# Performance work log

Hardware: AMD Instinct MI355X
Metric: run time of the kernel (lower is better)

The kernel has to match this reference:

```python
import jax, jax.numpy as jnp
import numpy as np

N, E, F, H, C = 50000, 800000, 128, 256, 40
BN_EPS = 1e-5


def setup_inputs() -> dict:
    key = jax.random.key(0)
    ks = jax.random.split(key, 8)
    s = 0.05
    return {
        'x': jax.random.normal(ks[0], (N, F), jnp.float32),
        'edge_index': jax.random.randint(ks[1], (2, E), 0, N),
        'eps1': jnp.zeros((), jnp.float32),
        'W1': jax.random.normal(ks[2], (F, H), jnp.float32) * s,
        'b1': jnp.zeros((H,), jnp.float32),
        'g1': jnp.ones((H,), jnp.float32),
        'be1': jnp.zeros((H,), jnp.float32),
        'W2': jax.random.normal(ks[3], (H, H), jnp.float32) * s,
        'b2': jnp.zeros((H,), jnp.float32),
        'eps2': jnp.zeros((), jnp.float32),
        'W3': jax.random.normal(ks[4], (H, H), jnp.float32) * s,
        'b3': jnp.zeros((H,), jnp.float32),
        'g2': jnp.ones((H,), jnp.float32),
        'be2': jnp.zeros((H,), jnp.float32),
        'W4': jax.random.normal(ks[5], (H, H), jnp.float32) * s,
        'b4': jnp.zeros((H,), jnp.float32),
        'g3': jnp.ones((H,), jnp.float32),
        'be3': jnp.zeros((H,), jnp.float32),
        'Wf': jax.random.normal(ks[6], (H, C), jnp.float32) * s,
        'bf': jnp.zeros((C,), jnp.float32),
    }


def _bn(h, g, b):
    # BatchNorm1d forward with batch statistics (training-mode math, biased var)
    m = jnp.mean(h, axis=0)
    v = jnp.var(h, axis=0)
    return (h - m) * jax.lax.rsqrt(v + BN_EPS) * g + b


def _gin_conv(x, edge_index, eps, Wa, ba, g, be, Wb, bb):
    # GINConv: out = mlp((1+eps)*x + sum_{(src->dst)} x[src])
    src, dst = edge_index[0], edge_index[1]
    agg = jax.ops.segment_sum(x[src], dst, num_segments=x.shape[0])  # [N, d]
    h = (1.0 + eps) * x + agg
    h = jnp.maximum(_bn(h @ Wa + ba, g, be), 0.0)  # Linear-BN-ReLU
    return h @ Wb + bb                              # Linear


def reference(x, edge_index, eps1, W1, b1, g1, be1, W2, b2,
              eps2, W3, b3, g2, be2, W4, b4, g3, be3, Wf, bf):
    h = _gin_conv(x, edge_index, eps1, W1, b1, g1, be1, W2, b2)
    h = jnp.maximum(h, 0.0)  # F.relu (dropout p=0)
    h = _gin_conv(h, edge_index, eps2, W3, b3, g2, be2, W4, b4)
    h = jnp.maximum(_bn(h, g3, be3), 0.0)  # bn2 + relu
    return h @ Wf + bf  # fc -> [N, C]
```

## Files before the change

### kernel.cpp

```cpp
#include <hip/hip_runtime.h>
#include <hip/hip_bf16.h>


#define NN 50000
#define EE 800000
#define FDIM 128
#define HDIM 256
#define CDIM 40
#define BN_EPS 1e-5f

typedef unsigned short u16;
typedef unsigned int u32;
typedef __attribute__((ext_vector_type(8))) short short8;
typedef __attribute__((ext_vector_type(4))) float f32x4;

__device__ __forceinline__ float bflo(u32 u) { return __uint_as_float(u << 16); }
__device__ __forceinline__ float bfhi(u32 u) { return __uint_as_float(u & 0xFFFF0000u); }
__device__ __forceinline__ u16 f2bf(float f) {
  __hip_bfloat16 h = __float2bfloat16(f);
  return *(u16*)&h;
}
__device__ __forceinline__ u32 pack2(float a, float b) {
  return (u32)f2bf(a) | ((u32)f2bf(b) << 16);
}

__global__ void k_scan_blocks(const int* __restrict__ in, int* __restrict__ partial,
                              int* __restrict__ bsums, int n) {
  __shared__ int s[256];
  int i = blockIdx.x * 256 + threadIdx.x;
  s[threadIdx.x] = (i < n) ? in[i] : 0;
  __syncthreads();
  for (int d = 1; d < 256; d <<= 1) {
    int t = (threadIdx.x >= d) ? s[threadIdx.x - d] : 0;
    __syncthreads();
    s[threadIdx.x] += t;
    __syncthreads();
  }
  if (i < n) partial[i] = s[threadIdx.x];
  if (threadIdx.x == 255) bsums[blockIdx.x] = s[255];
}

__global__ void k_scan_sums(int* __restrict__ bs, int nb) {
  __shared__ int s[256];
  s[threadIdx.x] = (threadIdx.x < nb) ? bs[threadIdx.x] : 0;
  __syncthreads();
  for (int d = 1; d < 256; d <<= 1) {
    int t = (threadIdx.x >= d) ? s[threadIdx.x - d] : 0;
    __syncthreads();
    s[threadIdx.x] += t;
    __syncthreads();
  }
  int ex = (threadIdx.x == 0) ? 0 : s[threadIdx.x - 1];
  if (threadIdx.x < nb) bs[threadIdx.x] = ex;
}

__global__ void k_scan_add(const int* __restrict__ partial, const int* __restrict__ bs,
                           const int* __restrict__ deg,
                           int* __restrict__ rowstart, int* __restrict__ cursor, int n) {
  int i = blockIdx.x * 256 + threadIdx.x;
  if (i < n) {
    int incl = partial[i] + bs[blockIdx.x];
    rowstart[i + 1] = incl;
    cursor[i] = incl - deg[i];
  }
  if (i == 0) rowstart[0] = 0;
}

#define SC_CHUNK 1024
#define SC_NCHUNK ((EE + SC_CHUNK - 1) / SC_CHUNK)
#define SC_NWIN 8
#define SC_WINSZ 6250
__global__ __launch_bounds__(256)
void k_scatter(const int* __restrict__ ei, int* __restrict__ cursor,
               int* __restrict__ sorted_src) {
  int win = blockIdx.x & (SC_NWIN - 1);
  int chunk = blockIdx.x >> 3;
  int wlo = win * SC_WINSZ, whi = wlo + SC_WINSZ;
  int e0 = chunk * SC_CHUNK + threadIdx.x * 4;
  if (e0 >= EE) return;
  int4 s4 = *(const int4*)&ei[e0];
  int4 d4 = *(const int4*)&ei[EE + e0];
  int ss[4] = {s4.x, s4.y, s4.z, s4.w};
  int dd[4] = {d4.x, d4.y, d4.z, d4.w};
#pragma unroll
  for (int i = 0; i < 4; ++i) {
    if (dd[i] >= wlo && dd[i] < whi) {
      int p = atomicAdd(&cursor[dd[i]], 1);
      sorted_src[p] = ss[i];
    }
  }
}

#define NB_CVTX 6250
#define NB_CVTW 944
#define NB_HIST 3125
__global__ void k_pre(const float* __restrict__ x, u16* __restrict__ xb,
                      const int* __restrict__ ei, int* __restrict__ deg,
                      const float* __restrict__ W1, const float* __restrict__ W2,
                      const float* __restrict__ W3, const float* __restrict__ W4,
                      const float* __restrict__ Wf,
                      u16* __restrict__ W1t, u16* __restrict__ W2t,
                      u16* __restrict__ W3t, u16* __restrict__ W4t,
                      u16* __restrict__ Wft) {
  int b = blockIdx.x, t = threadIdx.x;
  if (b < NB_CVTX) {
    size_t base = ((size_t)b * 256 + t) * 4;
    float4 v = *(const float4*)&x[base];
    *(uint2*)&xb[base] = make_uint2(pack2(v.x, v.y), pack2(v.z, v.w));
  } else if (b < NB_CVTX + NB_CVTW) {
    int bb = b - NB_CVTX;
    if (bb < 128) {
      int i = bb * 256 + t; int k = i >> 8, n = i & 255;
      W1t[(size_t)n * 128 + (((k >> 3) ^ (n & 7)) << 3) + (k & 7)] = f2bf(W1[i]);
    } else if (bb < 384) {
      int i = (bb - 128) * 256 + t; int k = i >> 8, n = i & 255;
      W2t[(size_t)n * 256 + (((k >> 3) ^ (n & 7)) << 3) + (k & 7)] = f2bf(W2[i]);
    } else if (bb < 640) {
      int i = (bb - 384) * 256 + t; int k = i >> 8, n = i & 255;
      W3t[(size_t)n * 256 + (((k >> 3) ^ (n & 7)) << 3) + (k & 7)] = f2bf(W3[i]);
    } else if (bb < 896) {
      int i = (bb - 640) * 256 + t; int k = i >> 8, n = i & 255;
      W4t[(size_t)n * 256 + (((k >> 3) ^ (n & 7)) << 3) + (k & 7)] = f2bf(W4[i]);
    } else {
      int j = (bb - 896) * 256 + t;
      int c = j >> 8, k = j & 255;
      float v = (c < CDIM) ? Wf[(size_t)k * CDIM + c] : 0.f;
      Wft[(size_t)c * 256 + (((k >> 3) ^ (c & 7)) << 3) + (k & 7)] = f2bf(v);
    }
  } else {
    int e = (b - NB_CVTX - NB_CVTW) * 256 + t;
    atomicAdd(&deg[ei[EE + e]], 1);
  }
}

template <int FEAT>
__global__ __launch_bounds__(256)
void k_agg(const u16* __restrict__ x, const int* __restrict__ rowstart,
           const int* __restrict__ sorted_src, const float* __restrict__ epsp,
           u16* __restrict__ out) {
  int node = blockIdx.x * 4 + (threadIdx.x >> 6);
  if (node >= NN) return;
  int lane = threadIdx.x & 63;
  float e1 = 1.0f + epsp[0];
  int s = rowstart[node], t = rowstart[node + 1];
  if constexpr (FEAT == 128) {
    const u32* xp = (const u32*)x;
    u32 u = xp[(size_t)node * 64 + lane];
    float a0 = bflo(u) * e1, a1 = bfhi(u) * e1;
    int p = s;
    for (; p + 7 < t; p += 8) {
      u32 uu[8];
#pragma unroll
      for (int i = 0; i < 8; ++i) uu[i] = xp[(size_t)sorted_src[p + i] * 64 + lane];
#pragma unroll
      for (int i = 0; i < 8; ++i) { a0 += bflo(uu[i]); a1 += bfhi(uu[i]); }
    }
    for (; p < t; ++p) {
      u32 u0 = xp[(size_t)sorted_src[p] * 64 + lane];
      a0 += bflo(u0); a1 += bfhi(u0);
    }
    ((u32*)out)[(size_t)node * 64 + lane] = pack2(a0, a1);
  } else {
    const uint2* xp = (const uint2*)x;
    uint2 u = xp[(size_t)node * 64 + lane];
    float a0 = bflo(u.x) * e1, a1 = bfhi(u.x) * e1;
    float a2 = bflo(u.y) * e1, a3 = bfhi(u.y) * e1;
    int p = s;
    for (; p + 7 < t; p += 8) {
      uint2 uu[8];
#pragma unroll
      for (int i = 0; i < 8; ++i) uu[i] = xp[(size_t)sorted_src[p + i] * 64 + lane];
#pragma unroll
      for (int i = 0; i < 8; ++i) {
        a0 += bflo(uu[i].x); a1 += bfhi(uu[i].x);
        a2 += bflo(uu[i].y); a3 += bfhi(uu[i].y);
      }
    }
    for (; p < t; ++p) {
      uint2 u0 = xp[(size_t)sorted_src[p] * 64 + lane];
      a0 += bflo(u0.x); a1 += bfhi(u0.x);
      a2 += bflo(u0.y); a3 += bfhi(u0.y);
    }
    ((uint2*)out)[(size_t)node * 64 + lane] = make_uint2(pack2(a0, a1), pack2(a2, a3));
  }
}

template <int K, bool TRANSFORM, bool RELU_OUT, bool COLSUMS>
__global__ __launch_bounds__(512, 4)
void k_gemm(const u16* __restrict__ A, const u16* __restrict__ Wt,
            const float* __restrict__ bias,
            const float* __restrict__ icsum, const float* __restrict__ icsq,
            const float* __restrict__ g, const float* __restrict__ be,
            u16* __restrict__ C, float* __restrict__ ocsum, float* __restrict__ ocsq) {
  __shared__ u16 SMEM[128 * 64 + 256 * 64];
  __shared__ float2 Tb[TRANSFORM ? 256 : 1];
  u16* Asm = SMEM;
  u16* Bsm = SMEM + 128 * 64;

  const int tid = threadIdx.x;
  const int lane = tid & 63;
  const int w = tid >> 6;
  const int wm = w >> 2, wn = w & 3;
  const int lr = lane & 15, lq = lane >> 4;
  const int r0 = blockIdx.x * 128;

  if constexpr (TRANSFORM) {
    if (tid < 256) {
      float m = icsum[tid] * (1.0f / NN);
      float var = icsq[tid] * (1.0f / NN) - m * m;
      float s = g[tid] * rsqrtf(var + BN_EPS);
      Tb[tid] = make_float2(s, be[tid] - m * s);
    }
    __syncthreads();
  }

  f32x4 acc[4][4];
#pragma unroll
  for (int mi = 0; mi < 4; ++mi)
#pragma unroll
    for (int ni = 0; ni < 4; ++ni) acc[mi][ni] = (f32x4){0.f, 0.f, 0.f, 0.f};

  const int srow = tid >> 3;
  const int sc = tid & 7;

  short8 pa[2];
  auto LOADA = [&](int k0) {
#pragma unroll
    for (int it = 0; it < 2; ++it) {
      int gr = r0 + it * 64 + srow;
      int grc = gr < NN ? gr : NN - 1;
      pa[it] = *(const short8*)&A[(size_t)grc * K + k0 + sc * 8];
    }
  };

  LOADA(0);
  for (int k0 = 0; k0 < K; k0 += 64) {
    if (k0 > 0) __syncthreads();
#pragma unroll
    for (int it = 0; it < 2; ++it) {
      int row = it * 64 + srow;
      short8 va = pa[it];
      if constexpr (TRANSFORM) {
#pragma unroll
        for (int j = 0; j < 8; ++j) {
          float2 tb = Tb[k0 + sc * 8 + j];
          float f = fmaxf(fmaf(__uint_as_float(((u32)(u16)va[j]) << 16), tb.x, tb.y), 0.f);
          va[j] = (short)f2bf(f);
        }
      }
      ((short8*)Asm)[row * 8 + (sc ^ (row & 7))] = va;
    }
#pragma unroll
    for (int it = 0; it < 4; ++it) {
      int row = it * 64 + srow;
      short8 vb = *(const short8*)&Wt[(size_t)row * K + k0 + sc * 8];
      ((short8*)Bsm)[row * 8 + sc] = vb;
    }
    if (k0 + 64 < K) LOADA(k0 + 64);
    __syncthreads();

#pragma unroll
    for (int ks = 0; ks < 2; ++ks) {
      short8 af[4], bfx[4];
#pragma unroll
      for (int mi = 0; mi < 4; ++mi) {
        int row = wm * 64 + mi * 16 + lr;
        af[mi] = ((const short8*)Asm)[row * 8 + ((ks * 4 + lq) ^ (row & 7))];
      }
#pragma unroll
      for (int ni = 0; ni < 4; ++ni) {
        int rn = wn * 64 + ni * 16 + lr;
        bfx[ni] = ((const short8*)Bsm)[rn * 8 + ((ks * 4 + lq) ^ (rn & 7))];
      }
#pragma unroll
      for (int mi = 0; mi < 4; ++mi)
#pragma unroll
        for (int ni = 0; ni < 4; ++ni)
          acc[mi][ni] = __builtin_amdgcn_mfma_f32_16x16x32_bf16(af[mi], bfx[ni], acc[mi][ni], 0, 0, 0);
    }
  }
  __syncthreads();

  float bv[4];
#pragma unroll
  for (int ni = 0; ni < 4; ++ni) bv[ni] = bias[wn * 64 + ni * 16 + lr];
  float colS[4] = {}, colQ[4] = {};

  u16* Cs = SMEM;
#pragma unroll
  for (int r = 0; r < 2; ++r) {
    if (wm == r) {
#pragma unroll
      for (int mi = 0; mi < 4; ++mi)
#pragma unroll
        for (int ni = 0; ni < 4; ++ni) {
          int col = wn * 64 + ni * 16 + lr;
#pragma unroll
          for (int j = 0; j < 4; ++j) {
            int lrow = mi * 16 + lq * 4 + j;
            float v = acc[mi][ni][j] + bv[ni];
            if constexpr (RELU_OUT) v = fmaxf(v, 0.f);
            if constexpr (COLSUMS) {
              if (r0 + r * 64 + lrow < NN) { colS[ni] += v; colQ[ni] += v * v; }
            }
            Cs[lrow * 256 + col] = f2bf(v);
          }
        }
    }
    __syncthreads();
    {
      int lrow = tid >> 3;
      int gr = r0 + r * 64 + lrow;
      if (gr < NN) {
        int co = (tid & 7) * 32;
#pragma unroll
        for (int i = 0; i < 4; ++i)
          *(uint4*)&C[(size_t)gr * 256 + co + i * 8] = *(const uint4*)&Cs[lrow * 256 + co + i * 8];
      }
    }
    __syncthreads();
  }

  if constexpr (COLSUMS) {
#pragma unroll
    for (int ni = 0; ni < 4; ++ni) {
      float s = colS[ni], q = colQ[ni];
      s += __shfl_xor(s, 16); s += __shfl_xor(s, 32);
      q += __shfl_xor(q, 16); q += __shfl_xor(q, 32);
      if (lq == 0) {
        int col = wn * 64 + ni * 16 + lr;
        atomicAdd(&ocsum[col], s);
        atomicAdd(&ocsq[col], q);
      }
    }
  }
}

__global__ __launch_bounds__(512)
void k_final(const u16* __restrict__ z3, const u16* __restrict__ Wft,
             const float* __restrict__ bfp,
             const float* __restrict__ icsum, const float* __restrict__ icsq,
             const float* __restrict__ g, const float* __restrict__ be,
             float* __restrict__ out) {
  __shared__ u16 Bs[48 * 256];
  __shared__ float2 Tb[256];
  const int tid = threadIdx.x;
  const int lane = tid & 63;
  const int w = tid >> 6;
  const int lr = lane & 15, lq = lane >> 4;
  const int r0 = blockIdx.x * 128;

  int row = r0 + w * 16 + lr;
  int rc = row < NN ? row : NN - 1;
  const u16* Ap = &z3[(size_t)rc * 256];
  short8 a[8];
#pragma unroll
  for (int ks = 0; ks < 8; ++ks)
    a[ks] = *(const short8*)&Ap[(ks * 4 + lq) * 8];

  {
    const short8* Bv = (const short8*)Wft;
    short8* Bl = (short8*)Bs;
#pragma unroll
    for (int i = 0; i < 3; ++i)
      Bl[tid + i * 512] = Bv[tid + i * 512];
  }
  if (tid < 256) {
    float m = icsum[tid] * (1.0f / NN);
    float var = icsq[tid] * (1.0f / NN) - m * m;
    float s = g[tid] * rsqrtf(var + BN_EPS);
    Tb[tid] = make_float2(s, be[tid] - m * s);
  }
  __syncthreads();

  f32x4 acc[3];
#pragma unroll
  for (int ni = 0; ni < 3; ++ni) acc[ni] = (f32x4){0.f, 0.f, 0.f, 0.f};
#pragma unroll
  for (int ks = 0; ks < 8; ++ks) {
    short8 t0 = a[ks];
    int kb = (ks * 4 + lq) * 8;
#pragma unroll
    for (int j = 0; j < 8; ++j) {
      float2 tb = Tb[kb + j];
      float f0 = fmaxf(fmaf(__uint_as_float(((u32)(u16)t0[j]) << 16), tb.x, tb.y), 0.f);
      t0[j] = (short)f2bf(f0);
    }
#pragma unroll
    for (int ni = 0; ni < 3; ++ni) {
      int col = ni * 16 + lr;
      short8 bfr = *(const short8*)&Bs[(size_t)col * 256 + (((ks * 4 + lq) ^ (col & 7)) << 3)];
      acc[ni] = __builtin_amdgcn_mfma_f32_16x16x32_bf16(t0, bfr, acc[ni], 0, 0, 0);
    }
  }

#pragma unroll
  for (int ni = 0; ni < 3; ++ni) {
    int col = ni * 16 + lr;
    if (col < CDIM) {
      float bfv = bfp[col];
#pragma unroll
      for (int j = 0; j < 4; ++j) {
        int gr = r0 + w * 16 + lq * 4 + j;
        if (gr < NN) out[(size_t)gr * CDIM + col] = acc[ni][j] + bfv;
      }
    }
  }
}

extern "C" void kernel_launch(void* const* d_in, const int* in_sizes, int n_in,
                              void* d_out, int out_size, void* d_ws, size_t ws_size,
                              hipStream_t stream) {
  const float* x   = (const float*)d_in[0];
  const int*   ei  = (const int*)d_in[1];
  const float* eps1= (const float*)d_in[2];
  const float* W1  = (const float*)d_in[3];
  const float* b1  = (const float*)d_in[4];
  const float* g1  = (const float*)d_in[5];
  const float* be1 = (const float*)d_in[6];
  const float* W2  = (const float*)d_in[7];
  const float* b2  = (const float*)d_in[8];
  const float* eps2= (const float*)d_in[9];
  const float* W3  = (const float*)d_in[10];
  const float* b3  = (const float*)d_in[11];
  const float* g2  = (const float*)d_in[12];
  const float* be2 = (const float*)d_in[13];
  const float* W4  = (const float*)d_in[14];
  const float* b4  = (const float*)d_in[15];
  const float* g3  = (const float*)d_in[16];
  const float* be3 = (const float*)d_in[17];
  const float* Wf  = (const float*)d_in[18];
  const float* bf  = (const float*)d_in[19];
  float* out = (float*)d_out;

  char* p = (char*)d_ws;
  auto alloc = [&](size_t bytes) -> char* {
    char* r = p;
    p += (bytes + 255) & ~(size_t)255;
    return r;
  };
  float* stats   = (float*)alloc(6 * 256 * sizeof(float));
  int* deg       = (int*)alloc(NN * sizeof(int));
  int* rowstart  = (int*)alloc((NN + 16) * sizeof(int));
  int* cursor    = (int*)alloc(NN * sizeof(int));
  int* sorted    = (int*)alloc(EE * sizeof(int));
  int* partial   = (int*)alloc(NN * sizeof(int));
  int* bsums     = (int*)alloc(1024 * sizeof(int));
  u16* W1t       = (u16*)alloc(256 * 128 * sizeof(u16));
  u16* W2t       = (u16*)alloc(256 * 256 * sizeof(u16));
  u16* W3t       = (u16*)alloc(256 * 256 * sizeof(u16));
  u16* W4t       = (u16*)alloc(256 * 256 * sizeof(u16));
  u16* Wft       = (u16*)alloc(48 * 256 * sizeof(u16));
  u16* xb        = (u16*)alloc((size_t)NN * 128 * sizeof(u16));
  u16* A1        = (u16*)alloc((size_t)NN * 128 * sizeof(u16));
  u16* z1        = (u16*)alloc((size_t)NN * 256 * sizeof(u16));
  u16* h1        = (u16*)alloc((size_t)NN * 256 * sizeof(u16));
  u16* A2        = (u16*)alloc((size_t)NN * 256 * sizeof(u16));
  (void)alloc(64 * 1024);
  u16* z2 = z1;
  u16* z3 = h1;

  float* s1 = stats + 0,    *q1 = stats + 256;
  float* s2 = stats + 512,  *q2 = stats + 768;
  float* s3 = stats + 1024, *q3 = stats + 1280;

  const int nbN = (NN + 255) / 256;

  hipMemsetAsync(stats, 0, 6 * 256 * sizeof(float) + NN * sizeof(int), stream);

  k_pre<<<NB_CVTX + NB_CVTW + NB_HIST, 256, 0, stream>>>(
      x, xb, ei, deg, W1, W2, W3, W4, Wf, W1t, W2t, W3t, W4t, Wft);
  k_scan_blocks<<<nbN, 256, 0, stream>>>(deg, partial, bsums, NN);
  k_scan_sums<<<1, 256, 0, stream>>>(bsums, nbN);
  k_scan_add<<<nbN, 256, 0, stream>>>(partial, bsums, deg, rowstart, cursor, NN);
  k_scatter<<<SC_NCHUNK * SC_NWIN, 256, 0, stream>>>(ei, cursor, sorted);

  const int gGemm = (NN + 127) / 128;

  k_agg<128><<<(NN + 3) / 4, 256, 0, stream>>>(xb, rowstart, sorted, eps1, A1);
  k_gemm<128, false, false, true><<<gGemm, 512, 0, stream>>>(
      A1, W1t, b1, nullptr, nullptr, nullptr, nullptr, z1, s1, q1);
  k_gemm<256, true, true, false><<<gGemm, 512, 0, stream>>>(
      z1, W2t, b2, s1, q1, g1, be1, h1, nullptr, nullptr);

  k_agg<256><<<(NN + 3) / 4, 256, 0, stream>>>(h1, rowstart, sorted, eps2, A2);
  k_gemm<256, false, false, true><<<gGemm, 512, 0, stream>>>(
      A2, W3t, b3, nullptr, nullptr, nullptr, nullptr, z2, s2, q2);
  k_gemm<256, true, false, true><<<gGemm, 512, 0, stream>>>(
      z2, W4t, b4, s2, q2, g2, be2, z3, s3, q3);

  k_final<<<(NN + 127) / 128, 512, 0, stream>>>(z3, Wft, bf, s3, q3, g3, be3, out);
}
```

Before: 328.6 us.

## Double-buffer GEMM shared-memory tiles with K=32 steps and register prefetch

Restructures the GEMM main loop from 64-wide K tiles in a single shared buffer to 32-wide K slices in two ping-pong A/B buffers. The next slice's global loads are issued before the MFMAs and written to the alternate buffer afterwards, so one barrier per step replaces two. The weight pre-transpose drops its XOR swizzle; the kernel now reads weights row-major and applies its own 4-chunk swizzle when storing to shared memory. Each step does fewer MFMAs between barriers, so synchronisation overhead per unit of work may rise.

```diff
diff --git a/kernel.cpp b/kernel.cpp
--- a/kernel.cpp
+++ b/kernel.cpp
@@ -111,16 +111,16 @@
     int bb = b - NB_CVTX;
     if (bb < 128) {
       int i = bb * 256 + t; int k = i >> 8, n = i & 255;
-      W1t[(size_t)n * 128 + (((k >> 3) ^ (n & 7)) << 3) + (k & 7)] = f2bf(W1[i]);
+      W1t[(size_t)n * 128 + k] = f2bf(W1[i]);
     } else if (bb < 384) {
       int i = (bb - 128) * 256 + t; int k = i >> 8, n = i & 255;
-      W2t[(size_t)n * 256 + (((k >> 3) ^ (n & 7)) << 3) + (k & 7)] = f2bf(W2[i]);
+      W2t[(size_t)n * 256 + k] = f2bf(W2[i]);
     } else if (bb < 640) {
       int i = (bb - 384) * 256 + t; int k = i >> 8, n = i & 255;
-      W3t[(size_t)n * 256 + (((k >> 3) ^ (n & 7)) << 3) + (k & 7)] = f2bf(W3[i]);
+      W3t[(size_t)n * 256 + k] = f2bf(W3[i]);
     } else if (bb < 896) {
       int i = (bb - 640) * 256 + t; int k = i >> 8, n = i & 255;
-      W4t[(size_t)n * 256 + (((k >> 3) ^ (n & 7)) << 3) + (k & 7)] = f2bf(W4[i]);
+      W4t[(size_t)n * 256 + k] = f2bf(W4[i]);
     } else {
       int j = (bb - 896) * 256 + t;
       int c = j >> 8, k = j & 255;
@@ -192,10 +192,9 @@
             const float* __restrict__ icsum, const float* __restrict__ icsq,
             const float* __restrict__ g, const float* __restrict__ be,
             u16* __restrict__ C, float* __restrict__ ocsum, float* __restrict__ ocsq) {
-  __shared__ u16 SMEM[128 * 64 + 256 * 64];
+  constexpr int NKS = K / 32;
+  __shared__ u16 SMEM[2 * 128 * 32 + 2 * 256 * 32];
   __shared__ float2 Tb[TRANSFORM ? 256 : 1];
-  u16* Asm = SMEM;
-  u16* Bsm = SMEM + 128 * 64;
 
   const int tid = threadIdx.x;
   const int lane = tid & 63;
@@ -204,6 +203,11 @@
   const int lr = lane & 15, lq = lane >> 4;
   const int r0 = blockIdx.x * 128;
 
+  u16* const Ab0 = SMEM;
+  u16* const Ab1 = SMEM + 128 * 32;
+  u16* const Bb0 = SMEM + 2 * 128 * 32;
+  u16* const Bb1 = SMEM + 2 * 128 * 32 + 256 * 32;
+
   if constexpr (TRANSFORM) {
     if (tid < 256) {
       float m = icsum[tid] * (1.0f / NN);
@@ -214,72 +218,77 @@
     __syncthreads();
   }
 
+  const int arow = tid >> 2, ach = tid & 3;
+  const int agrc = (r0 + arow) < NN ? (r0 + arow) : NN - 1;
+  const int b1r = (tid + 512) >> 2;
+
+  auto WRA = [&](u16* buf, short8 v, int ks) {
+    if constexpr (TRANSFORM) {
+#pragma unroll
+      for (int j = 0; j < 8; ++j) {
+        float2 tb = Tb[ks * 32 + ach * 8 + j];
+        float f = fmaxf(fmaf(__uint_as_float(((u32)(u16)v[j]) << 16), tb.x, tb.y), 0.f);
+        v[j] = (short)f2bf(f);
+      }
+    }
+    ((short8*)buf)[arow * 4 + (ach ^ ((arow >> 1) & 3))] = v;
+  };
+  auto WRB = [&](u16* buf, short8 v, int row) {
+    ((short8*)buf)[row * 4 + (ach ^ ((row >> 1) & 3))] = v;
+  };
+
   f32x4 acc[4][4];
 #pragma unroll
   for (int mi = 0; mi < 4; ++mi)
 #pragma unroll
     for (int ni = 0; ni < 4; ++ni) acc[mi][ni] = (f32x4){0.f, 0.f, 0.f, 0.f};
 
-  const int srow = tid >> 3;
-  const int sc = tid & 7;
-
-  short8 pa[2];
-  auto LOADA = [&](int k0) {
-#pragma unroll
-    for (int it = 0; it < 2; ++it) {
-      int gr = r0 + it * 64 + srow;
-      int grc = gr < NN ? gr : NN - 1;
-      pa[it] = *(const short8*)&A[(size_t)grc * K + k0 + sc * 8];
-    }
-  };
-
-  LOADA(0);
-  for (int k0 = 0; k0 < K; k0 += 64) {
-    if (k0 > 0) __syncthreads();
-#pragma unroll
-    for (int it = 0; it < 2; ++it) {
-      int row = it * 64 + srow;
-      short8 va = pa[it];
-      if constexpr (TRANSFORM) {
-#pragma unroll
-        for (int j = 0; j < 8; ++j) {
-          float2 tb = Tb[k0 + sc * 8 + j];
-          float f = fmaxf(fmaf(__uint_as_float(((u32)(u16)va[j]) << 16), tb.x, tb.y), 0.f);
-          va[j] = (short)f2bf(f);
-        }
-      }
-      ((short8*)Asm)[row * 8 + (sc ^ (row & 7))] = va;
-    }
-#pragma unroll
-    for (int it = 0; it < 4; ++it) {
-      int row = it * 64 + srow;
-      short8 vb = *(const short8*)&Wt[(size_t)row * K + k0 + sc * 8];
-      ((short8*)Bsm)[row * 8 + sc] = vb;
-    }
-    if (k0 + 64 < K) LOADA(k0 + 64);
-    __syncthreads();
-
-#pragma unroll
-    for (int ks = 0; ks < 2; ++ks) {
-      short8 af[4], bfx[4];
-#pragma unroll
-      for (int mi = 0; mi < 4; ++mi) {
-        int row = wm * 64 + mi * 16 + lr;
-        af[mi] = ((const short8*)Asm)[row * 8 + ((ks * 4 + lq) ^ (row & 7))];
-      }
-#pragma unroll
-      for (int ni = 0; ni < 4; ++ni) {
-        int rn = wn * 64 + ni * 16 + lr;
-        bfx[ni] = ((const short8*)Bsm)[rn * 8 + ((ks * 4 + lq) ^ (rn & 7))];
-      }
-#pragma unroll
-      for (int mi = 0; mi < 4; ++mi)
-#pragma unroll
-        for (int ni = 0; ni < 4; ++ni)
-          acc[mi][ni] = __builtin_amdgcn_mfma_f32_16x16x32_bf16(af[mi], bfx[ni], acc[mi][ni], 0, 0, 0);
-    }
+  {
+    short8 ra  = *(const short8*)&A[(size_t)agrc * K + ach * 8];
+    short8 rb0 = *(const short8*)&Wt[(size_t)arow * K + ach * 8];
+    short8 rb1 = *(const short8*)&Wt[(size_t)b1r * K + ach * 8];
+    WRA(Ab0, ra, 0);
+    WRB(Bb0, rb0, arow);
+    WRB(Bb0, rb1, b1r);
   }
   __syncthreads();
+
+#pragma unroll
+  for (int ks = 0; ks < NKS; ++ks) {
+    short8 na = (short8)0, nb0 = (short8)0, nb1 = (short8)0;
+    if (ks + 1 < NKS) {
+      int ko = (ks + 1) * 32 + ach * 8;
+      na  = *(const short8*)&A[(size_t)agrc * K + ko];
+      nb0 = *(const short8*)&Wt[(size_t)arow * K + ko];
+      nb1 = *(const short8*)&Wt[(size_t)b1r * K + ko];
+    }
+    const u16* Ab = (ks & 1) ? Ab1 : Ab0;
+    const u16* Bb = (ks & 1) ? Bb1 : Bb0;
+    short8 af[4], bfx[4];
+#pragma unroll
+    for (int mi = 0; mi < 4; ++mi) {
+      int row = wm * 64 + mi * 16 + lr;
+      af[mi] = ((const short8*)Ab)[row * 4 + (lq ^ ((row >> 1) & 3))];
+    }
+#pragma unroll
+    for (int ni = 0; ni < 4; ++ni) {
+      int rn = wn * 64 + ni * 16 + lr;
+      bfx[ni] = ((const short8*)Bb)[rn * 4 + (lq ^ ((rn >> 1) & 3))];
+    }
+#pragma unroll
+    for (int mi = 0; mi < 4; ++mi)
+#pragma unroll
+      for (int ni = 0; ni < 4; ++ni)
+        acc[mi][ni] = __builtin_amdgcn_mfma_f32_16x16x32_bf16(af[mi], bfx[ni], acc[mi][ni], 0, 0, 0);
+    if (ks + 1 < NKS) {
+      u16* An = (ks & 1) ? Ab0 : Ab1;
+      u16* Bn = (ks & 1) ? Bb0 : Bb1;
+      WRA(An, na, ks + 1);
+      WRB(Bn, nb0, arow);
+      WRB(Bn, nb1, b1r);
+    }
+    __syncthreads();
+  }
 
   float bv[4];
 #pragma unroll
```

New measurement: 324.3 us. Within noise of the previous version (-1.3%).
